# Kernel tuning notes

Hardware: AMD Instinct MI355X
Metric: run time of the kernel (lower is better)

## Reference

```python
import jax, jax.numpy as jnp
import numpy as np

EMBED_DIM = 128
TANH_CLIP = 10.0


def setup_inputs() -> dict:
    key = jax.random.key(0)
    k1, k2, k3, k4 = jax.random.split(key, 4)
    B, NA, NC, D = 64, 100, 5000, EMBED_DIM
    agent_embed = jax.random.normal(k1, (B, NA, D), dtype=jnp.float32)
    city_embed = jax.random.normal(k2, (B, NC, D), dtype=jnp.float32)
    scale = 1.0 / np.sqrt(D)
    Wq = jax.random.uniform(k3, (D, D), dtype=jnp.float32, minval=-scale, maxval=scale)
    Wk = jax.random.uniform(k4, (D, D), dtype=jnp.float32, minval=-scale, maxval=scale)
    return {"agent_embed": agent_embed, "city_embed": city_embed, "Wq": Wq, "Wk": Wk}


def reference(agent_embed, city_embed, Wq, Wk):
    # SingleHeadAttention: q from city_embed (query), k from agent_embed (key)
    D = Wq.shape[0]
    q = jnp.einsum('bcd,de->bce', city_embed, Wq)   # [B, n_city, D]
    k = jnp.einsum('bad,de->bae', agent_embed, Wk)  # [B, n_agent, D]
    scores = jnp.einsum('bcd,bad->bca', q, k) / jnp.sqrt(jnp.asarray(D, q.dtype))
    compat = TANH_CLIP * jnp.tanh(scores)           # [B, n_city, n_agent]
    agent = jnp.argmax(compat, axis=-1)             # [B, n_city] int
    return agent
```

## Files before the change

kernel.cpp:

```cpp
#include <hip/hip_runtime.h>

#define DIM     128
#define NAGENT  100
#define NAP     112
#define NCITY   5000
#define NBATCH  64
#define NA_PAD  101
#define SUSP_CAP 16384
#define EPS     2e-3f

#define CPB     128
#define CTILES  ((NCITY + CPB - 1) / CPB)
#define FRAG_PB 14336
#define CHUNKS  3584

#define OFF_CNT 0
#define OFF_SUS 512
#define OFF_KP  66048
#define OFF_GF  3342848

typedef __attribute__((ext_vector_type(8))) short short8;
typedef __attribute__((ext_vector_type(4))) float f32x4;

__device__ __forceinline__ unsigned short bf16_rne(float x) {
    unsigned u = __float_as_uint(x);
    u += 0x7FFFu + ((u >> 16) & 1u);
    return (unsigned short)(u >> 16);
}
__device__ __forceinline__ float bf16_tof(unsigned short h) {
    return __uint_as_float(((unsigned)h) << 16);
}

__global__ __launch_bounds__(128) void proj_k_kernel(const float* __restrict__ agent,
                                                     const float* __restrict__ Wk,
                                                     float* __restrict__ kp32,
                                                     int* __restrict__ counter) {
    const int ba = blockIdx.x;
    const int e  = threadIdx.x;

    if (ba == 0 && e == 0) *counter = 0;

    __shared__ float s_a[DIM];
    s_a[e] = agent[(size_t)ba * DIM + e];
    __syncthreads();

    double a0 = 0.0, a1 = 0.0, a2 = 0.0, a3 = 0.0;
    #pragma unroll 8
    for (int d = 0; d < DIM; d += 4) {
        a0 += (double)s_a[d + 0] * (double)Wk[(d + 0) * DIM + e];
        a1 += (double)s_a[d + 1] * (double)Wk[(d + 1) * DIM + e];
        a2 += (double)s_a[d + 2] * (double)Wk[(d + 2) * DIM + e];
        a3 += (double)s_a[d + 3] * (double)Wk[(d + 3) * DIM + e];
    }
    kp32[(size_t)ba * DIM + e] = (float)((a0 + a1) + (a2 + a3));
}

__global__ __launch_bounds__(256) void gmat_kernel(const float* __restrict__ Wq,
                                                   const float* __restrict__ kp32,
                                                   unsigned short* __restrict__ Gf) {
    const int b      = blockIdx.x >> 3;
    const int dchunk = blockIdx.x & 7;
    const int tid    = threadIdx.x;

    __shared__ float s_kp[DIM][NA_PAD];

    const float* kpb = kp32 + (size_t)b * NAGENT * DIM;
    for (int i = tid; i < NAGENT * DIM; i += 256) {
        int a = i >> 7;
        int e = i & 127;
        s_kp[e][a] = kpb[i];
    }
    __syncthreads();

    unsigned short* GfB = Gf + (size_t)b * (2 * FRAG_PB);
    const int d0 = dchunk * 16;
    for (int i = tid; i < 16 * NAP; i += 256) {
        int dl = i / NAP;
        int a  = i - dl * NAP;
        int d  = d0 + dl;
        unsigned short hi = 0, lo = 0;
        if (a < NAGENT) {
            const float* wq = Wq + d * DIM;
            double q0 = 0.0, q1 = 0.0, q2 = 0.0, q3 = 0.0;
            #pragma unroll 8
            for (int e = 0; e < DIM; e += 4) {
                q0 += (double)wq[e + 0] * (double)s_kp[e + 0][a];
                q1 += (double)wq[e + 1] * (double)s_kp[e + 1][a];
                q2 += (double)wq[e + 2] * (double)s_kp[e + 2][a];
                q3 += (double)wq[e + 3] * (double)s_kp[e + 3][a];
            }
            float g = (float)((q0 + q1) + (q2 + q3));
            hi = bf16_rne(g);
            lo = bf16_rne(g - bf16_tof(hi));
        }
        int t = a >> 4, col = a & 15;
        int ks = d >> 5, kgrp = (d >> 3) & 3, j = d & 7;
        int fidx = (((t * 4 + ks) * 64) + (kgrp * 16 + col)) * 8 + j;
        GfB[fidx] = hi;
        GfB[FRAG_PB + fidx] = lo;
    }
}

__global__ __launch_bounds__(512)
void score_mfma_kernel(const float* __restrict__ city,
                       const unsigned short* __restrict__ Gf,
                       int* __restrict__ out,
                       int* __restrict__ counter,
                       int* __restrict__ suspects) {
    const int b    = blockIdx.x / CTILES;
    const int ct   = blockIdx.x % CTILES;
    const int tid  = threadIdx.x;
    const int wave = tid >> 6;
    const int lane = tid & 63;
    const int col  = lane & 15;
    const int kgrp = lane >> 4;

    __shared__ short8 s_frag[CHUNKS];

    {
        const char* gsrc = (const char*)(Gf + (size_t)b * (2 * FRAG_PB));
        #pragma unroll
        for (int it = 0; it < CHUNKS / 512; ++it) {
            int chunk = it * 512 + tid;
            __builtin_amdgcn_global_load_lds(
                (const __attribute__((address_space(1))) unsigned int*)(gsrc + (size_t)chunk * 16),
                (__attribute__((address_space(3))) unsigned int*)((char*)s_frag + (it * 512 + wave * 64) * 16),
                16, 0, 0);
        }
    }

    const int c0 = ct * CPB + wave * 16;
    int crow = c0 + col; if (crow > NCITY - 1) crow = NCITY - 1;
    const float* crp = city + ((size_t)b * NCITY + crow) * DIM + kgrp * 8;

    short8 aHi[4], aLo[4];
    #pragma unroll
    for (int ks = 0; ks < 4; ++ks) {
        float4 p0 = *(const float4*)(crp + ks * 32);
        float4 p1 = *(const float4*)(crp + ks * 32 + 4);
        float f[8] = {p0.x, p0.y, p0.z, p0.w, p1.x, p1.y, p1.z, p1.w};
        short8 h, l;
        #pragma unroll
        for (int j = 0; j < 8; ++j) {
            unsigned short hb = bf16_rne(f[j]);
            h[j] = (short)hb;
            l[j] = (short)bf16_rne(f[j] - bf16_tof(hb));
        }
        aHi[ks] = h;
        aLo[ks] = l;
    }

    __syncthreads();

    f32x4 acc[7];
    #pragma unroll
    for (int t = 0; t < 7; ++t) {
        f32x4 a4 = {0.f, 0.f, 0.f, 0.f};
        #pragma unroll
        for (int ks = 0; ks < 4; ++ks) {
            int fi = (t * 4 + ks) * 64 + lane;
            short8 bH = s_frag[fi];
            short8 bL = s_frag[1792 + fi];
            a4 = __builtin_amdgcn_mfma_f32_16x16x32_bf16(aHi[ks], bH, a4, 0, 0, 0);
            a4 = __builtin_amdgcn_mfma_f32_16x16x32_bf16(aHi[ks], bL, a4, 0, 0, 0);
            a4 = __builtin_amdgcn_mfma_f32_16x16x32_bf16(aLo[ks], bH, a4, 0, 0, 0);
        }
        acc[t] = a4;
    }

    #pragma unroll
    for (int r = 0; r < 4; ++r) {
        float b1 = -1e30f, b2 = -1e30f; int i1 = 0x7fffffff;
        #pragma unroll
        for (int t = 0; t < 7; ++t) {
            int a  = t * 16 + col;
            float v = (a < NAGENT) ? acc[t][r] : -1e30f;
            if (v > b1)      { b2 = b1; b1 = v; i1 = a; }
            else if (v > b2) { b2 = v; }
        }
        #pragma unroll
        for (int m = 1; m <= 8; m <<= 1) {
            float ob1 = __shfl_xor(b1, m);
            int   oi1 = __shfl_xor(i1, m);
            float ob2 = __shfl_xor(b2, m);
            if (ob1 > b1 || (ob1 == b1 && oi1 < i1)) {
                b2 = fmaxf(b1, ob2); b1 = ob1; i1 = oi1;
            } else {
                b2 = fmaxf(b2, ob1);
            }
        }
        if (col == 0) {
            int c = c0 + kgrp * 4 + r;
            if (c < NCITY) {
                int bc = b * NCITY + c;
                out[bc] = i1;
                if (b1 - b2 < EPS) {
                    int s = atomicAdd(counter, 1);
                    if (s < SUSP_CAP) suspects[s] = bc;
                }
            }
        }
    }
}

__global__ __launch_bounds__(128) void recheck_kernel(const float* __restrict__ city,
                                                      const float* __restrict__ agent,
                                                      const float* __restrict__ Wq,
                                                      const float* __restrict__ Wk,
                                                      const int* __restrict__ counter,
                                                      const int* __restrict__ suspects,
                                                      int* __restrict__ out) {
    int n = *counter;
    if (n > SUSP_CAP) n = SUSP_CAP;
    const int e = threadIdx.x;

    __shared__ float  s_c[DIM];
    __shared__ double s_q[DIM];
    __shared__ double s_r[DIM];
    __shared__ double s_best[DIM];
    __shared__ int    s_bidx[DIM];

    for (int s = blockIdx.x; s < n; s += gridDim.x) {
        const int bc = suspects[s];
        const int b  = bc / NCITY;

        s_c[e] = city[(size_t)bc * DIM + e];
        __syncthreads();

        double q = 0.0;
        #pragma unroll 8
        for (int d = 0; d < DIM; ++d)
            q += (double)s_c[d] * (double)Wq[d * DIM + e];
        s_q[e] = q;
        __syncthreads();

        double r = 0.0;
        #pragma unroll 8
        for (int k = 0; k < DIM; ++k)
            r += (double)Wk[e * DIM + k] * s_q[k];
        s_r[e] = r;
        __syncthreads();

        double best = -1.0e300;
        int    bidx = 0x7fffffff;
        if (e < NAGENT) {
            const float* ar = agent + ((size_t)b * NAGENT + e) * DIM;
            double sc = 0.0;
            #pragma unroll 8
            for (int d = 0; d < DIM; ++d)
                sc += (double)ar[d] * s_r[d];
            best = sc; bidx = e;
        }
        s_best[e] = best; s_bidx[e] = bidx;
        __syncthreads();

        for (int off = 64; off > 0; off >>= 1) {
            if (e < off) {
                double ov = s_best[e + off];
                int    oi = s_bidx[e + off];
                if (ov > s_best[e] || (ov == s_best[e] && oi < s_bidx[e])) {
                    s_best[e] = ov; s_bidx[e] = oi;
                }
            }
            __syncthreads();
        }
        if (e == 0) out[bc] = s_bidx[0];
        __syncthreads();
    }
}

extern "C" void kernel_launch(void* const* d_in, const int* in_sizes, int n_in,
                              void* d_out, int out_size, void* d_ws, size_t ws_size,
                              hipStream_t stream) {
    const float* agent = (const float*)d_in[0];
    const float* city  = (const float*)d_in[1];
    const float* Wq    = (const float*)d_in[2];
    const float* Wk    = (const float*)d_in[3];
    int* out = (int*)d_out;

    char*           ws       = (char*)d_ws;
    int*            counter  = (int*)(ws + OFF_CNT);
    int*            suspects = (int*)(ws + OFF_SUS);
    float*          kp32     = (float*)(ws + OFF_KP);
    unsigned short* Gf       = (unsigned short*)(ws + OFF_GF);

    proj_k_kernel<<<NBATCH * NAGENT, DIM, 0, stream>>>(agent, Wk, kp32, counter);
    gmat_kernel<<<NBATCH * 8, 256, 0, stream>>>(Wq, kp32, Gf);
    score_mfma_kernel<<<NBATCH * CTILES, 512, 0, stream>>>(city, Gf, out, counter, suspects);
    recheck_kernel<<<1024, DIM, 0, stream>>>(city, agent, Wq, Wk, counter, suspects, out);
}
```

Before: 106.4 us.

## Make score kernel persistent over city tiles with prefetch; fp32 projections

The score kernel now launches 8 blocks per batch, and each block loops over 5 city tiles. The per-batch G fragment is loaded into LDS once per block instead of once per tile, and the next tile's city rows are loaded and split into bf16 hi/lo while the current tile's argmax epilogue runs. The bf16 split of city values uses a cheaper round-half-up hi and a truncated lo. The two projection kernels switch from double to float FMA accumulation. The float accumulation and cheaper rounding reduce precision, which could produce more near-tie suspects for the recheck kernel or change some argmax results.

```diff
diff --git a/kernel.cpp b/kernel.cpp
--- a/kernel.cpp
+++ b/kernel.cpp
@@ -11,6 +11,8 @@
 
 #define CPB     128
 #define CTILES  ((NCITY + CPB - 1) / CPB)
+#define NT      5
+#define BPB     8
 #define FRAG_PB 14336
 #define CHUNKS  3584
 
@@ -44,15 +46,15 @@
     s_a[e] = agent[(size_t)ba * DIM + e];
     __syncthreads();
 
-    double a0 = 0.0, a1 = 0.0, a2 = 0.0, a3 = 0.0;
+    float a0 = 0.f, a1 = 0.f, a2 = 0.f, a3 = 0.f;
     #pragma unroll 8
     for (int d = 0; d < DIM; d += 4) {
-        a0 += (double)s_a[d + 0] * (double)Wk[(d + 0) * DIM + e];
-        a1 += (double)s_a[d + 1] * (double)Wk[(d + 1) * DIM + e];
-        a2 += (double)s_a[d + 2] * (double)Wk[(d + 2) * DIM + e];
-        a3 += (double)s_a[d + 3] * (double)Wk[(d + 3) * DIM + e];
-    }
-    kp32[(size_t)ba * DIM + e] = (float)((a0 + a1) + (a2 + a3));
+        a0 = fmaf(s_a[d + 0], Wk[(d + 0) * DIM + e], a0);
+        a1 = fmaf(s_a[d + 1], Wk[(d + 1) * DIM + e], a1);
+        a2 = fmaf(s_a[d + 2], Wk[(d + 2) * DIM + e], a2);
+        a3 = fmaf(s_a[d + 3], Wk[(d + 3) * DIM + e], a3);
+    }
+    kp32[(size_t)ba * DIM + e] = (a0 + a1) + (a2 + a3);
 }
 
 __global__ __launch_bounds__(256) void gmat_kernel(const float* __restrict__ Wq,
@@ -81,15 +83,15 @@
         unsigned short hi = 0, lo = 0;
         if (a < NAGENT) {
             const float* wq = Wq + d * DIM;
-            double q0 = 0.0, q1 = 0.0, q2 = 0.0, q3 = 0.0;
+            float q0 = 0.f, q1 = 0.f, q2 = 0.f, q3 = 0.f;
             #pragma unroll 8
             for (int e = 0; e < DIM; e += 4) {
-                q0 += (double)wq[e + 0] * (double)s_kp[e + 0][a];
-                q1 += (double)wq[e + 1] * (double)s_kp[e + 1][a];
-                q2 += (double)wq[e + 2] * (double)s_kp[e + 2][a];
-                q3 += (double)wq[e + 3] * (double)s_kp[e + 3][a];
-            }
-            float g = (float)((q0 + q1) + (q2 + q3));
+                q0 = fmaf(wq[e + 0], s_kp[e + 0][a], q0);
+                q1 = fmaf(wq[e + 1], s_kp[e + 1][a], q1);
+                q2 = fmaf(wq[e + 2], s_kp[e + 2][a], q2);
+                q3 = fmaf(wq[e + 3], s_kp[e + 3][a], q3);
+            }
+            float g = (q0 + q1) + (q2 + q3);
             hi = bf16_rne(g);
             lo = bf16_rne(g - bf16_tof(hi));
         }
@@ -101,14 +103,36 @@
     }
 }
 
-__global__ __launch_bounds__(512)
+__device__ __forceinline__ void load_split_A(const float* __restrict__ crp,
+                                             short8* aHi, short8* aLo) {
+    #pragma unroll
+    for (int ks = 0; ks < 4; ++ks) {
+        float4 p0 = *(const float4*)(crp + ks * 32);
+        float4 p1 = *(const float4*)(crp + ks * 32 + 4);
+        float f[8] = {p0.x, p0.y, p0.z, p0.w, p1.x, p1.y, p1.z, p1.w};
+        short8 h, l;
+        #pragma unroll
+        for (int j = 0; j < 8; ++j) {
+            unsigned ur = __float_as_uint(f[j]) + 0x8000u;
+            h[j] = (short)(ur >> 16);
+            float hif = __uint_as_float(ur & 0xFFFF0000u);
+            float lo  = f[j] - hif;
+            l[j] = (short)(__float_as_uint(lo) >> 16);
+        }
+        aHi[ks] = h;
+        aLo[ks] = l;
+    }
+}
+
+__global__ __launch_bounds__(512, 4)
 void score_mfma_kernel(const float* __restrict__ city,
                        const unsigned short* __restrict__ Gf,
                        int* __restrict__ out,
                        int* __restrict__ counter,
                        int* __restrict__ suspects) {
-    const int b    = blockIdx.x / CTILES;
-    const int ct   = blockIdx.x % CTILES;
+    const int b    = blockIdx.x / BPB;
+    const int bi   = blockIdx.x % BPB;
+    const int ct0  = bi * NT;
     const int tid  = threadIdx.x;
     const int wave = tid >> 6;
     const int lane = tid & 63;
@@ -129,76 +153,80 @@
         }
     }
 
-    const int c0 = ct * CPB + wave * 16;
-    int crow = c0 + col; if (crow > NCITY - 1) crow = NCITY - 1;
-    const float* crp = city + ((size_t)b * NCITY + crow) * DIM + kgrp * 8;
-
-    short8 aHi[4], aLo[4];
-    #pragma unroll
-    for (int ks = 0; ks < 4; ++ks) {
-        float4 p0 = *(const float4*)(crp + ks * 32);
-        float4 p1 = *(const float4*)(crp + ks * 32 + 4);
-        float f[8] = {p0.x, p0.y, p0.z, p0.w, p1.x, p1.y, p1.z, p1.w};
-        short8 h, l;
-        #pragma unroll
-        for (int j = 0; j < 8; ++j) {
-            unsigned short hb = bf16_rne(f[j]);
-            h[j] = (short)hb;
-            l[j] = (short)bf16_rne(f[j] - bf16_tof(hb));
-        }
-        aHi[ks] = h;
-        aLo[ks] = l;
+    const float* cityb = city + (size_t)b * NCITY * DIM;
+
+    short8 aHi[4], aLo[4], nHi[4], nLo[4];
+    {
+        int crow = ct0 * CPB + wave * 16 + col;
+        if (crow > NCITY - 1) crow = NCITY - 1;
+        load_split_A(cityb + (size_t)crow * DIM + kgrp * 8, aHi, aLo);
     }
 
     __syncthreads();
 
-    f32x4 acc[7];
-    #pragma unroll
-    for (int t = 0; t < 7; ++t) {
-        f32x4 a4 = {0.f, 0.f, 0.f, 0.f};
-        #pragma unroll
-        for (int ks = 0; ks < 4; ++ks) {
-            int fi = (t * 4 + ks) * 64 + lane;
-            short8 bH = s_frag[fi];
-            short8 bL = s_frag[1792 + fi];
-            a4 = __builtin_amdgcn_mfma_f32_16x16x32_bf16(aHi[ks], bH, a4, 0, 0, 0);
-            a4 = __builtin_amdgcn_mfma_f32_16x16x32_bf16(aHi[ks], bL, a4, 0, 0, 0);
-            a4 = __builtin_amdgcn_mfma_f32_16x16x32_bf16(aLo[ks], bH, a4, 0, 0, 0);
-        }
-        acc[t] = a4;
-    }
-
-    #pragma unroll
-    for (int r = 0; r < 4; ++r) {
-        float b1 = -1e30f, b2 = -1e30f; int i1 = 0x7fffffff;
+    for (int it = 0; it < NT; ++it) {
+        const int ct = ct0 + it;
+        const int c0 = ct * CPB + wave * 16;
+
+        f32x4 acc[7];
         #pragma unroll
         for (int t = 0; t < 7; ++t) {
-            int a  = t * 16 + col;
-            float v = (a < NAGENT) ? acc[t][r] : -1e30f;
-            if (v > b1)      { b2 = b1; b1 = v; i1 = a; }
-            else if (v > b2) { b2 = v; }
-        }
+            f32x4 a4 = {0.f, 0.f, 0.f, 0.f};
+            #pragma unroll
+            for (int ks = 0; ks < 4; ++ks) {
+                int fi = (t * 4 + ks) * 64 + lane;
+                short8 bH = s_frag[fi];
+                short8 bL = s_frag[1792 + fi];
+                a4 = __builtin_amdgcn_mfma_f32_16x16x32_bf16(aHi[ks], bH, a4, 0, 0, 0);
+                a4 = __builtin_amdgcn_mfma_f32_16x16x32_bf16(aHi[ks], bL, a4, 0, 0, 0);
+                a4 = __builtin_amdgcn_mfma_f32_16x16x32_bf16(aLo[ks], bH, a4, 0, 0, 0);
+            }
+            acc[t] = a4;
+        }
+
+        if (it + 1 < NT) {
+            int crow = (ct + 1) * CPB + wave * 16 + col;
+            if (crow > NCITY - 1) crow = NCITY - 1;
+            load_split_A(cityb + (size_t)crow * DIM + kgrp * 8, nHi, nLo);
+        }
+
         #pragma unroll
-        for (int m = 1; m <= 8; m <<= 1) {
-            float ob1 = __shfl_xor(b1, m);
-            int   oi1 = __shfl_xor(i1, m);
-            float ob2 = __shfl_xor(b2, m);
-            if (ob1 > b1 || (ob1 == b1 && oi1 < i1)) {
-                b2 = fmaxf(b1, ob2); b1 = ob1; i1 = oi1;
-            } else {
-                b2 = fmaxf(b2, ob1);
-            }
-        }
-        if (col == 0) {
-            int c = c0 + kgrp * 4 + r;
-            if (c < NCITY) {
-                int bc = b * NCITY + c;
-                out[bc] = i1;
-                if (b1 - b2 < EPS) {
-                    int s = atomicAdd(counter, 1);
-                    if (s < SUSP_CAP) suspects[s] = bc;
+        for (int r = 0; r < 4; ++r) {
+            float b1 = -1e30f, b2 = -1e30f; int i1 = 0x7fffffff;
+            #pragma unroll
+            for (int t = 0; t < 7; ++t) {
+                int a  = t * 16 + col;
+                float v = (a < NAGENT) ? acc[t][r] : -1e30f;
+                if (v > b1)      { b2 = b1; b1 = v; i1 = a; }
+                else if (v > b2) { b2 = v; }
+            }
+            #pragma unroll
+            for (int m = 1; m <= 8; m <<= 1) {
+                float ob1 = __shfl_xor(b1, m);
+                int   oi1 = __shfl_xor(i1, m);
+                float ob2 = __shfl_xor(b2, m);
+                if (ob1 > b1 || (ob1 == b1 && oi1 < i1)) {
+                    b2 = fmaxf(b1, ob2); b1 = ob1; i1 = oi1;
+                } else {
+                    b2 = fmaxf(b2, ob1);
                 }
             }
+            if (col == 0) {
+                int c = c0 + kgrp * 4 + r;
+                if (c < NCITY) {
+                    int bc = b * NCITY + c;
+                    out[bc] = i1;
+                    if (b1 - b2 < EPS) {
+                        int s = atomicAdd(counter, 1);
+                        if (s < SUSP_CAP) suspects[s] = bc;
+                    }
+                }
+            }
+        }
+
+        if (it + 1 < NT) {
+            #pragma unroll
+            for (int ks = 0; ks < 4; ++ks) { aHi[ks] = nHi[ks]; aLo[ks] = nLo[ks]; }
         }
     }
 }
@@ -286,6 +314,6 @@
 
     proj_k_kernel<<<NBATCH * NAGENT, DIM, 0, stream>>>(agent, Wk, kp32, counter);
     gmat_kernel<<<NBATCH * 8, 256, 0, stream>>>(Wq, kp32, Gf);
-    score_mfma_kernel<<<NBATCH * CTILES, 512, 0, stream>>>(city, Gf, out, counter, suspects);
+    score_mfma_kernel<<<NBATCH * BPB, 512, 0, stream>>>(city, Gf, out, counter, suspects);
     recheck_kernel<<<1024, DIM, 0, stream>>>(city, agent, Wq, Wk, counter, suspects, out);
 }
```

New measurement: 300.8 us. 2.83x slower.
